# Kernel tuning notes

Measured on AMD Instinct MI355X. Metric: run time of the kernel, lower is better.

The kernel has to match this reference:

```python
import jax, jax.numpy as jnp
import numpy as np

N_NODES = 50000
N_EDGES = 800000
N_FEAT = 16
N_BASIS = 4
GAMMA = 10.0
R_MAX = 5.0
INV_SQRT2 = 0.7071067811865476


def setup_inputs() -> dict:
    key = jax.random.key(0)
    k1, k2, k3, k4 = jax.random.split(key, 4)
    pos = jax.random.normal(k1, (N_NODES, 3), dtype=jnp.float32)
    node_features = jax.random.normal(k2, (N_NODES, N_FEAT), dtype=jnp.float32)
    # build edges with no self-loops: dst = (src + 1 + r) % N, r in [0, N-2]
    src = jax.random.randint(k3, (N_EDGES,), 0, N_NODES)
    r = jax.random.randint(k4, (N_EDGES,), 0, N_NODES - 1)
    dst = (src + 1 + r) % N_NODES
    edge_idx = jnp.stack([src, dst], axis=0).astype(jnp.int64)
    return {"pos": pos, "node_features": node_features, "edge_idx": edge_idx}


def _gaussian_basis(d):
    # d: [E] -> [E, N_BASIS]
    centers = jnp.linspace(0.0, R_MAX, N_BASIS, dtype=d.dtype)
    return jnp.exp(-GAMMA * (d[:, None] - centers[None, :]) ** 2)


def _pos_to_rep(v):
    # v: [N, 3, C] cartesian along axis -2 -> complex spherical l=1 basis,
    # returned as stacked (real, imag): [2, N, 3, C]
    x, y, z = v[..., 0, :], v[..., 1, :], v[..., 2, :]
    zero = jnp.zeros_like(z)
    real = jnp.stack([x * INV_SQRT2, z, -x * INV_SQRT2], axis=-2)
    imag = jnp.stack([-y * INV_SQRT2, zero, -y * INV_SQRT2], axis=-2)
    return jnp.stack([real, imag], axis=0)


def reference(pos, node_features, edge_idx):
    src, dst = edge_idx[0], edge_idx[1]
    disp = pos[dst] - pos[src]                      # [E, 3]
    dist = jnp.linalg.norm(disp, axis=-1)           # [E]
    bf = _gaussian_basis(dist)                      # [E, B]
    unit = disp / dist[:, None]                     # [E, 3]
    nf = node_features[dst]                         # [E, F]
    # outer products: [E, 3, B, F]
    edge_vals = (unit[:, :, None, None] * bf[:, None, :, None]
                 * nf[:, None, None, :])
    edge_vals = edge_vals.reshape(edge_vals.shape[0], 3, N_BASIS * N_FEAT)
    node_vecs = jax.ops.segment_sum(edge_vals, src, num_segments=N_NODES)  # [N,3,C]
    return _pos_to_rep(node_vecs)
```

## Files before the change

kernel.cpp:

```cpp
#include <hip/hip_runtime.h>

#define N_FEAT 16
#define N_BASIS 4
#define GAMMA 10.0f
#define R_MAX 5.0f
#define INV_SQRT2 0.70710678118654752f

#define BUCKET 32
#define CAP 768
#define MAXB 2048
#define SC_BLOCK 512
#define SC_EDGES 4096
#define ACC_BLOCK 512

#define SLOTCAP 1280
#define ROWSTRIDE 1288

#define KC      (-GAMMA * 1.4426950408889634f)
#define CKD     (R_MAX / (N_BASIS - 1))

#if __has_builtin(__builtin_amdgcn_exp2f)
#define EXP2(x) __builtin_amdgcn_exp2f(x)
#else
#define EXP2(x) exp2f(x)
#endif

typedef _Float16 half8 __attribute__((ext_vector_type(8)));
typedef float f32x4 __attribute__((ext_vector_type(4)));

__global__ void bucket_scatter_kernel(const int* __restrict__ src,
                                      const int* __restrict__ dst,
                                      const float* __restrict__ pos,
                                      float4* __restrict__ pos4,
                                      int* __restrict__ gcursor,
                                      int* __restrict__ sorted,
                                      int n_edges, int nbuck, int n_nodes) {
    __shared__ int h[MAXB];
    __shared__ int cur[MAXB];
    __shared__ int gbase[MAXB];
    __shared__ int pay[SC_EDGES];

    int t = threadIdx.x;

    {
        int i = blockIdx.x * SC_BLOCK + t;
        if (i < n_nodes)
            pos4[i] = make_float4(pos[3 * i], pos[3 * i + 1], pos[3 * i + 2], 0.0f);
    }

    int base_e = blockIdx.x * SC_EDGES;
    int nloc = n_edges - base_e;
    if (nloc > SC_EDGES) nloc = SC_EDGES;

    for (int i = t; i < nbuck; i += SC_BLOCK) h[i] = 0;
    __syncthreads();

    unsigned pk[8];
    bool ok[8];
#pragma unroll
    for (int r = 0; r < 8; ++r) {
        int i = t + r * SC_BLOCK;
        ok[r] = (i < nloc);
        unsigned s = ok[r] ? (unsigned)src[base_e + i] : 0u;
        unsigned d = ok[r] ? (unsigned)dst[base_e + i] : 0u;
        pk[r] = (s << 16) | d;
        if (ok[r]) atomicAdd(&h[s >> 5], 1);
    }
    __syncthreads();

    if (t < 64) {
        int run = 0;
        for (int base = 0; base < nbuck; base += 64) {
            int i = base + t;
            int v = (i < nbuck) ? h[i] : 0;
            int incl = v;
            for (int off = 1; off < 64; off <<= 1) {
                int y = __shfl_up(incl, off, 64);
                if (t >= off) incl += y;
            }
            if (i < nbuck) h[i] = run + incl - v;
            run += __shfl(incl, 63, 64);
        }
    }
    __syncthreads();
    for (int i = t; i < nbuck; i += SC_BLOCK) cur[i] = h[i];
    __syncthreads();

#pragma unroll
    for (int r = 0; r < 8; ++r) {
        if (ok[r]) {
            int b = (int)(pk[r] >> 21);
            int p = atomicAdd(&cur[b], 1);
            pay[p] = (int)pk[r];
        }
    }
    __syncthreads();

    for (int b = t; b < nbuck; b += SC_BLOCK) {
        int c = cur[b] - h[b];
        gbase[b] = (c > 0) ? atomicAdd(&gcursor[b], c) : 0;
    }
    __syncthreads();

    for (int i = t; i < nloc; i += SC_BLOCK) {
        unsigned P = (unsigned)pay[i];
        int b = (int)(P >> 21);
        int idx = gbase[b] + (i - h[b]);
        if (idx < CAP) sorted[b * CAP + idx] = (int)P;
    }
}

__global__ __launch_bounds__(ACC_BLOCK) void accumulate_kernel(
        const float4* __restrict__ pos4,
        const float* __restrict__ nfeat,
        const int* __restrict__ sorted,
        const int* __restrict__ gcursor,
        float* __restrict__ out,
        int n_nodes) {
    __shared__ _Float16 a_lds[12 * ROWSTRIDE];
    __shared__ unsigned short slot_dst[SLOTCAP];
    __shared__ int cnt[BUCKET];
    __shared__ int soff[BUCKET];
    __shared__ int curs[BUCKET];
    __shared__ float4 spos[BUCKET];

    int b = blockIdx.x;
    int t = threadIdx.x;
    int w = t >> 6;
    int lane = t & 63;
    int q = lane >> 4;
    int f = lane & 15;
    int nbase = b << 5;

    int ecnt = gcursor[b];
    if (ecnt > CAP) ecnt = CAP;
    const int* seg = sorted + b * CAP;

    {
        int4 z4 = make_int4(0, 0, 0, 0);
        int4* az = (int4*)a_lds;
        for (int i = t; i < 1932; i += ACC_BLOCK) az[i] = z4;
        int4* sz = (int4*)slot_dst;
        if (t < 160) sz[t] = z4;
    }
    if (t < BUCKET) {
        cnt[t] = 0;
        int gn = nbase + t;
        spos[t] = (gn < n_nodes) ? pos4[gn] : make_float4(0.f, 0.f, 0.f, 0.f);
    }
    __syncthreads();

    for (int i = t; i < ecnt; i += ACC_BLOCK)
        atomicAdd(&cnt[((unsigned)seg[i] >> 16) & 31], 1);
    __syncthreads();

    if (t < BUCKET) {
        int deg = cnt[t];
        int pad = (deg + 31) & ~31;
        int incl = pad;
        for (int o2 = 1; o2 < BUCKET; o2 <<= 1) {
            int y = __shfl_up(incl, o2, 64);
            if (t >= o2) incl += y;
        }
        int excl = incl - pad;
        soff[t] = excl;
        curs[t] = excl;
    }
    __syncthreads();

    if (ecnt > 0) {
        int ecm1 = ecnt - 1;
        int i0 = t, i1 = t + ACC_BLOCK;
        bool v0 = (i0 < ecnt), v1 = (i1 < ecnt);
        unsigned E0 = (unsigned)seg[min(i0, ecm1)];
        unsigned E1 = (unsigned)seg[min(i1, ecm1)];
        int d0 = E0 & 0xFFFF, d1 = E1 & 0xFFFF;
        float4 pd0 = pos4[d0];
        float4 pd1 = pos4[d1];
        int sl0 = (E0 >> 16) & 31, sl1 = (E1 >> 16) & 31;
        int p0 = v0 ? atomicAdd(&curs[sl0], 1) : SLOTCAP;
        int p1 = v1 ? atomicAdd(&curs[sl1], 1) : SLOTCAP;

#define STAGE(P, SL, D, PD)                                            \
        if ((P) < SLOTCAP) {                                           \
            float4 ps = spos[SL];                                      \
            float dx = (PD).x - ps.x, dy = (PD).y - ps.y,              \
                  dz = (PD).z - ps.z;                                  \
            float r2 = dx * dx + dy * dy + dz * dz;                    \
            float inv = __builtin_amdgcn_rsqf(r2);                     \
            float dist = r2 * inv;                                     \
            float ux = dx * inv, uy = dy * inv, uz = dz * inv;         \
            slot_dst[P] = (unsigned short)(D);                         \
            _Float16* ap = a_lds + (P);                                \
            _Pragma("unroll")                                          \
            for (int kk = 0; kk < N_BASIS; ++kk) {                     \
                float ck = (float)kk * CKD;                            \
                float tt = dist - ck;                                  \
                float bb = EXP2(tt * tt * KC);                         \
                ap[kk * ROWSTRIDE]       = (_Float16)(ux * bb);        \
                ap[(4 + kk) * ROWSTRIDE] = (_Float16)(uy * bb);        \
                ap[(8 + kk) * ROWSTRIDE] = (_Float16)(uz * bb);        \
            }                                                          \
        }
        { STAGE(p0, sl0, d0, pd0); }
        if (v1) { STAGE(p1, sl1, d1, pd1); }
#undef STAGE
    }
    __syncthreads();

    int arow = (f < 12) ? f : 11;
    const _Float16* abase = &a_lds[arow * ROWSTRIDE];
#pragma unroll
    for (int half = 0; half < 2; ++half) {
        int nA = (w << 2) + (half << 1);
        int nB = nA + 1;
        int baseA = min(soff[nA], SLOTCAP - 32);
        int baseB = min(soff[nB], SLOTCAP - 32);
        int kA = baseA + (q << 3), kB = baseB + (q << 3);

        half8 aA = *(const half8*)&abase[kA];
        half8 aB = *(const half8*)&abase[kB];
        const unsigned short* dpA = &slot_dst[kA];
        const unsigned short* dpB = &slot_dst[kB];
        half8 bA, bB;
#pragma unroll
        for (int j = 0; j < 8; ++j) bA[j] = (_Float16)nfeat[((int)dpA[j] << 4) + f];
#pragma unroll
        for (int j = 0; j < 8; ++j) bB[j] = (_Float16)nfeat[((int)dpB[j] << 4) + f];

        f32x4 CA = {0.f, 0.f, 0.f, 0.f};
        f32x4 CB = {0.f, 0.f, 0.f, 0.f};
        CA = __builtin_amdgcn_mfma_f32_16x16x32_f16(aA, bA, CA, 0, 0, 0);
        CB = __builtin_amdgcn_mfma_f32_16x16x32_f16(aB, bB, CB, 0, 0, 0);

        int ntA = min((cnt[nA] + 31) >> 5, (SLOTCAP - baseA) >> 5);
        for (int tile = 1; tile < ntA; ++tile) {
            int k0 = baseA + (tile << 5) + (q << 3);
            half8 a = *(const half8*)&abase[k0];
            const unsigned short* dp = &slot_dst[k0];
            half8 bf;
#pragma unroll
            for (int j = 0; j < 8; ++j) bf[j] = (_Float16)nfeat[((int)dp[j] << 4) + f];
            CA = __builtin_amdgcn_mfma_f32_16x16x32_f16(a, bf, CA, 0, 0, 0);
        }
        int ntB = min((cnt[nB] + 31) >> 5, (SLOTCAP - baseB) >> 5);
        for (int tile = 1; tile < ntB; ++tile) {
            int k0 = baseB + (tile << 5) + (q << 3);
            half8 a = *(const half8*)&abase[k0];
            const unsigned short* dp = &slot_dst[k0];
            half8 bf;
#pragma unroll
            for (int j = 0; j < 8; ++j) bf[j] = (_Float16)nfeat[((int)dp[j] << 4) + f];
            CB = __builtin_amdgcn_mfma_f32_16x16x32_f16(a, bf, CB, 0, 0, 0);
        }

#define EPI(NL, C)                                                     \
        {                                                              \
            int gn = nbase + (NL);                                     \
            if (gn < n_nodes) {                                        \
                float* re = out + (size_t)gn * 192;                    \
                float* im = re + (size_t)n_nodes * 192;                \
                _Pragma("unroll")                                      \
                for (int r = 0; r < 4; ++r) {                          \
                    float v = (C)[r];                                  \
                    int o1 = r * 16 + f;                               \
                    if (q == 0) {                                      \
                        float xs = v * INV_SQRT2;                      \
                        re[o1] = xs;                                   \
                        re[128 + o1] = -xs;                            \
                    } else if (q == 1) {                               \
                        float ys = -v * INV_SQRT2;                     \
                        im[o1] = ys;                                   \
                        im[128 + o1] = ys;                             \
                    } else if (q == 2) {                               \
                        re[64 + o1] = v;                               \
                    } else {                                           \
                        im[64 + o1] = 0.0f;                            \
                    }                                                  \
                }                                                      \
            }                                                          \
        }
        EPI(nA, CA);
        EPI(nB, CB);
#undef EPI
    }
}

extern "C" void kernel_launch(void* const* d_in, const int* in_sizes, int n_in,
                              void* d_out, int out_size, void* d_ws, size_t ws_size,
                              hipStream_t stream) {
    const float* pos = (const float*)d_in[0];
    const float* nfeat = (const float*)d_in[1];
    const int* edge_idx = (const int*)d_in[2];

    int n_nodes = in_sizes[0] / 3;
    int n_edges = in_sizes[2] / 2;

    const int* src = edge_idx;
    const int* dst = edge_idx + n_edges;

    float* out = (float*)d_out;
    int nbuck = (n_nodes + BUCKET - 1) >> 5;

    char* ws = (char*)d_ws;
    size_t o = 0;
    auto alloc = [&](size_t bytes) {
        char* p = ws + o;
        o = (o + bytes + 255) & ~(size_t)255;
        return p;
    };
    int* gcursor = (int*)alloc((size_t)nbuck * 4);
    int* sorted  = (int*)alloc((size_t)nbuck * CAP * 4);
    float4* pos4 = (float4*)alloc((size_t)n_nodes * 16);

    (void)hipMemsetAsync(gcursor, 0, (size_t)nbuck * sizeof(int), stream);

    {
        int grid = (n_edges + SC_EDGES - 1) / SC_EDGES;
        bucket_scatter_kernel<<<grid, SC_BLOCK, 0, stream>>>(src, dst, pos, pos4,
                                                             gcursor, sorted,
                                                             n_edges, nbuck, n_nodes);
    }

    accumulate_kernel<<<nbuck, ACC_BLOCK, 0, stream>>>(pos4, nfeat, sorted, gcursor,
                                                       out, n_nodes);
}
```

Before: 59.18 us.

## Pre-convert node features to fp16 and make accumulate kernel persistent

The scatter kernel now also converts node features to an fp16 copy in workspace, so the accumulate kernel's gathers read 2-byte values and skip the per-element float-to-half conversion. The accumulate kernel becomes a grid-stride persistent loop over buckets with a fixed grid of 1024 blocks, adding a trailing barrier per iteration so the shared buffers can be reused. This halves gather traffic for the B operand at the cost of an extra write and read pass over the features, and it reduces block launch overhead but may cut latency hiding when fewer blocks are resident.

```diff
diff --git a/kernel.cpp b/kernel.cpp
--- a/kernel.cpp
+++ b/kernel.cpp
@@ -12,6 +12,7 @@
 #define SC_BLOCK 512
 #define SC_EDGES 4096
 #define ACC_BLOCK 512
+#define ACC_GRID 1024
 
 #define SLOTCAP 1280
 #define ROWSTRIDE 1288
@@ -31,7 +32,9 @@
 __global__ void bucket_scatter_kernel(const int* __restrict__ src,
                                       const int* __restrict__ dst,
                                       const float* __restrict__ pos,
+                                      const float* __restrict__ nfeat,
                                       float4* __restrict__ pos4,
+                                      _Float16* __restrict__ nf16,
                                       int* __restrict__ gcursor,
                                       int* __restrict__ sorted,
                                       int n_edges, int nbuck, int n_nodes) {
@@ -44,8 +47,23 @@
 
     {
         int i = blockIdx.x * SC_BLOCK + t;
-        if (i < n_nodes)
+        if (i < n_nodes) {
             pos4[i] = make_float4(pos[3 * i], pos[3 * i + 1], pos[3 * i + 2], 0.0f);
+            const float4* nfs = (const float4*)(nfeat + ((size_t)i << 4));
+            half8 lo, hi;
+            float4 v0 = nfs[0], v1 = nfs[1], v2 = nfs[2], v3 = nfs[3];
+            lo[0] = (_Float16)v0.x; lo[1] = (_Float16)v0.y;
+            lo[2] = (_Float16)v0.z; lo[3] = (_Float16)v0.w;
+            lo[4] = (_Float16)v1.x; lo[5] = (_Float16)v1.y;
+            lo[6] = (_Float16)v1.z; lo[7] = (_Float16)v1.w;
+            hi[0] = (_Float16)v2.x; hi[1] = (_Float16)v2.y;
+            hi[2] = (_Float16)v2.z; hi[3] = (_Float16)v2.w;
+            hi[4] = (_Float16)v3.x; hi[5] = (_Float16)v3.y;
+            hi[6] = (_Float16)v3.z; hi[7] = (_Float16)v3.w;
+            half8* dst16 = (half8*)(nf16 + ((size_t)i << 4));
+            dst16[0] = lo;
+            dst16[1] = hi;
+        }
     }
 
     int base_e = blockIdx.x * SC_EDGES;
@@ -112,11 +130,11 @@
 
 __global__ __launch_bounds__(ACC_BLOCK) void accumulate_kernel(
         const float4* __restrict__ pos4,
-        const float* __restrict__ nfeat,
+        const _Float16* __restrict__ nf16,
         const int* __restrict__ sorted,
         const int* __restrict__ gcursor,
         float* __restrict__ out,
-        int n_nodes) {
+        int n_nodes, int nbuck) {
     __shared__ _Float16 a_lds[12 * ROWSTRIDE];
     __shared__ unsigned short slot_dst[SLOTCAP];
     __shared__ int cnt[BUCKET];
@@ -124,165 +142,167 @@
     __shared__ int curs[BUCKET];
     __shared__ float4 spos[BUCKET];
 
-    int b = blockIdx.x;
     int t = threadIdx.x;
     int w = t >> 6;
     int lane = t & 63;
     int q = lane >> 4;
     int f = lane & 15;
-    int nbase = b << 5;
-
-    int ecnt = gcursor[b];
-    if (ecnt > CAP) ecnt = CAP;
-    const int* seg = sorted + b * CAP;
-
-    {
-        int4 z4 = make_int4(0, 0, 0, 0);
-        int4* az = (int4*)a_lds;
-        for (int i = t; i < 1932; i += ACC_BLOCK) az[i] = z4;
-        int4* sz = (int4*)slot_dst;
-        if (t < 160) sz[t] = z4;
-    }
-    if (t < BUCKET) {
-        cnt[t] = 0;
-        int gn = nbase + t;
-        spos[t] = (gn < n_nodes) ? pos4[gn] : make_float4(0.f, 0.f, 0.f, 0.f);
-    }
-    __syncthreads();
-
-    for (int i = t; i < ecnt; i += ACC_BLOCK)
-        atomicAdd(&cnt[((unsigned)seg[i] >> 16) & 31], 1);
-    __syncthreads();
-
-    if (t < BUCKET) {
-        int deg = cnt[t];
-        int pad = (deg + 31) & ~31;
-        int incl = pad;
-        for (int o2 = 1; o2 < BUCKET; o2 <<= 1) {
-            int y = __shfl_up(incl, o2, 64);
-            if (t >= o2) incl += y;
-        }
-        int excl = incl - pad;
-        soff[t] = excl;
-        curs[t] = excl;
-    }
-    __syncthreads();
-
-    if (ecnt > 0) {
-        int ecm1 = ecnt - 1;
-        int i0 = t, i1 = t + ACC_BLOCK;
-        bool v0 = (i0 < ecnt), v1 = (i1 < ecnt);
-        unsigned E0 = (unsigned)seg[min(i0, ecm1)];
-        unsigned E1 = (unsigned)seg[min(i1, ecm1)];
-        int d0 = E0 & 0xFFFF, d1 = E1 & 0xFFFF;
-        float4 pd0 = pos4[d0];
-        float4 pd1 = pos4[d1];
-        int sl0 = (E0 >> 16) & 31, sl1 = (E1 >> 16) & 31;
-        int p0 = v0 ? atomicAdd(&curs[sl0], 1) : SLOTCAP;
-        int p1 = v1 ? atomicAdd(&curs[sl1], 1) : SLOTCAP;
+    int arow = (f < 12) ? f : 11;
+
+    for (int b = blockIdx.x; b < nbuck; b += ACC_GRID) {
+        int nbase = b << 5;
+        int ecnt = gcursor[b];
+        if (ecnt > CAP) ecnt = CAP;
+        const int* seg = sorted + b * CAP;
+
+        {
+            int4 z4 = make_int4(0, 0, 0, 0);
+            int4* az = (int4*)a_lds;
+            for (int i = t; i < 1932; i += ACC_BLOCK) az[i] = z4;
+            int4* sz = (int4*)slot_dst;
+            if (t < 160) sz[t] = z4;
+        }
+        if (t < BUCKET) {
+            cnt[t] = 0;
+            int gn = nbase + t;
+            spos[t] = (gn < n_nodes) ? pos4[gn] : make_float4(0.f, 0.f, 0.f, 0.f);
+        }
+        __syncthreads();
+
+        for (int i = t; i < ecnt; i += ACC_BLOCK)
+            atomicAdd(&cnt[((unsigned)seg[i] >> 16) & 31], 1);
+        __syncthreads();
+
+        if (t < BUCKET) {
+            int deg = cnt[t];
+            int pad = (deg + 31) & ~31;
+            int incl = pad;
+            for (int o2 = 1; o2 < BUCKET; o2 <<= 1) {
+                int y = __shfl_up(incl, o2, 64);
+                if (t >= o2) incl += y;
+            }
+            int excl = incl - pad;
+            soff[t] = excl;
+            curs[t] = excl;
+        }
+        __syncthreads();
+
+        if (ecnt > 0) {
+            int ecm1 = ecnt - 1;
+            int i0 = t, i1 = t + ACC_BLOCK;
+            bool v0 = (i0 < ecnt), v1 = (i1 < ecnt);
+            unsigned E0 = (unsigned)seg[min(i0, ecm1)];
+            unsigned E1 = (unsigned)seg[min(i1, ecm1)];
+            int d0 = E0 & 0xFFFF, d1 = E1 & 0xFFFF;
+            float4 pd0 = pos4[d0];
+            float4 pd1 = pos4[d1];
+            int sl0 = (E0 >> 16) & 31, sl1 = (E1 >> 16) & 31;
+            int p0 = v0 ? atomicAdd(&curs[sl0], 1) : SLOTCAP;
+            int p1 = v1 ? atomicAdd(&curs[sl1], 1) : SLOTCAP;
 
 #define STAGE(P, SL, D, PD)                                            \
-        if ((P) < SLOTCAP) {                                           \
-            float4 ps = spos[SL];                                      \
-            float dx = (PD).x - ps.x, dy = (PD).y - ps.y,              \
-                  dz = (PD).z - ps.z;                                  \
-            float r2 = dx * dx + dy * dy + dz * dz;                    \
-            float inv = __builtin_amdgcn_rsqf(r2);                     \
-            float dist = r2 * inv;                                     \
-            float ux = dx * inv, uy = dy * inv, uz = dz * inv;         \
-            slot_dst[P] = (unsigned short)(D);                         \
-            _Float16* ap = a_lds + (P);                                \
-            _Pragma("unroll")                                          \
-            for (int kk = 0; kk < N_BASIS; ++kk) {                     \
-                float ck = (float)kk * CKD;                            \
-                float tt = dist - ck;                                  \
-                float bb = EXP2(tt * tt * KC);                         \
-                ap[kk * ROWSTRIDE]       = (_Float16)(ux * bb);        \
-                ap[(4 + kk) * ROWSTRIDE] = (_Float16)(uy * bb);        \
-                ap[(8 + kk) * ROWSTRIDE] = (_Float16)(uz * bb);        \
-            }                                                          \
-        }
-        { STAGE(p0, sl0, d0, pd0); }
-        if (v1) { STAGE(p1, sl1, d1, pd1); }
+            if ((P) < SLOTCAP) {                                       \
+                float4 ps = spos[SL];                                  \
+                float dx = (PD).x - ps.x, dy = (PD).y - ps.y,          \
+                      dz = (PD).z - ps.z;                              \
+                float r2 = dx * dx + dy * dy + dz * dz;                \
+                float inv = __builtin_amdgcn_rsqf(r2);                 \
+                float dist = r2 * inv;                                 \
+                float ux = dx * inv, uy = dy * inv, uz = dz * inv;     \
+                slot_dst[P] = (unsigned short)(D);                     \
+                _Float16* ap = a_lds + (P);                            \
+                _Pragma("unroll")                                      \
+                for (int kk = 0; kk < N_BASIS; ++kk) {                 \
+                    float ck = (float)kk * CKD;                        \
+                    float tt = dist - ck;                              \
+                    float bb = EXP2(tt * tt * KC);                     \
+                    ap[kk * ROWSTRIDE]       = (_Float16)(ux * bb);    \
+                    ap[(4 + kk) * ROWSTRIDE] = (_Float16)(uy * bb);    \
+                    ap[(8 + kk) * ROWSTRIDE] = (_Float16)(uz * bb);    \
+                }                                                      \
+            }
+            { STAGE(p0, sl0, d0, pd0); }
+            if (v1) { STAGE(p1, sl1, d1, pd1); }
 #undef STAGE
-    }
-    __syncthreads();
-
-    int arow = (f < 12) ? f : 11;
-    const _Float16* abase = &a_lds[arow * ROWSTRIDE];
-#pragma unroll
-    for (int half = 0; half < 2; ++half) {
-        int nA = (w << 2) + (half << 1);
-        int nB = nA + 1;
-        int baseA = min(soff[nA], SLOTCAP - 32);
-        int baseB = min(soff[nB], SLOTCAP - 32);
-        int kA = baseA + (q << 3), kB = baseB + (q << 3);
-
-        half8 aA = *(const half8*)&abase[kA];
-        half8 aB = *(const half8*)&abase[kB];
-        const unsigned short* dpA = &slot_dst[kA];
-        const unsigned short* dpB = &slot_dst[kB];
-        half8 bA, bB;
-#pragma unroll
-        for (int j = 0; j < 8; ++j) bA[j] = (_Float16)nfeat[((int)dpA[j] << 4) + f];
-#pragma unroll
-        for (int j = 0; j < 8; ++j) bB[j] = (_Float16)nfeat[((int)dpB[j] << 4) + f];
-
-        f32x4 CA = {0.f, 0.f, 0.f, 0.f};
-        f32x4 CB = {0.f, 0.f, 0.f, 0.f};
-        CA = __builtin_amdgcn_mfma_f32_16x16x32_f16(aA, bA, CA, 0, 0, 0);
-        CB = __builtin_amdgcn_mfma_f32_16x16x32_f16(aB, bB, CB, 0, 0, 0);
-
-        int ntA = min((cnt[nA] + 31) >> 5, (SLOTCAP - baseA) >> 5);
-        for (int tile = 1; tile < ntA; ++tile) {
-            int k0 = baseA + (tile << 5) + (q << 3);
-            half8 a = *(const half8*)&abase[k0];
-            const unsigned short* dp = &slot_dst[k0];
-            half8 bf;
-#pragma unroll
-            for (int j = 0; j < 8; ++j) bf[j] = (_Float16)nfeat[((int)dp[j] << 4) + f];
-            CA = __builtin_amdgcn_mfma_f32_16x16x32_f16(a, bf, CA, 0, 0, 0);
-        }
-        int ntB = min((cnt[nB] + 31) >> 5, (SLOTCAP - baseB) >> 5);
-        for (int tile = 1; tile < ntB; ++tile) {
-            int k0 = baseB + (tile << 5) + (q << 3);
-            half8 a = *(const half8*)&abase[k0];
-            const unsigned short* dp = &slot_dst[k0];
-            half8 bf;
-#pragma unroll
-            for (int j = 0; j < 8; ++j) bf[j] = (_Float16)nfeat[((int)dp[j] << 4) + f];
-            CB = __builtin_amdgcn_mfma_f32_16x16x32_f16(a, bf, CB, 0, 0, 0);
-        }
+        }
+        __syncthreads();
+
+        const _Float16* abase = &a_lds[arow * ROWSTRIDE];
+#pragma unroll
+        for (int half = 0; half < 2; ++half) {
+            int nA = (w << 2) + (half << 1);
+            int nB = nA + 1;
+            int baseA = min(soff[nA], SLOTCAP - 32);
+            int baseB = min(soff[nB], SLOTCAP - 32);
+            int kA = baseA + (q << 3), kB = baseB + (q << 3);
+
+            half8 aA = *(const half8*)&abase[kA];
+            half8 aB = *(const half8*)&abase[kB];
+            const unsigned short* dpA = &slot_dst[kA];
+            const unsigned short* dpB = &slot_dst[kB];
+            half8 bA, bB;
+#pragma unroll
+            for (int j = 0; j < 8; ++j) bA[j] = nf16[((int)dpA[j] << 4) + f];
+#pragma unroll
+            for (int j = 0; j < 8; ++j) bB[j] = nf16[((int)dpB[j] << 4) + f];
+
+            f32x4 CA = {0.f, 0.f, 0.f, 0.f};
+            f32x4 CB = {0.f, 0.f, 0.f, 0.f};
+            CA = __builtin_amdgcn_mfma_f32_16x16x32_f16(aA, bA, CA, 0, 0, 0);
+            CB = __builtin_amdgcn_mfma_f32_16x16x32_f16(aB, bB, CB, 0, 0, 0);
+
+            int ntA = min((cnt[nA] + 31) >> 5, (SLOTCAP - baseA) >> 5);
+            for (int tile = 1; tile < ntA; ++tile) {
+                int k0 = baseA + (tile << 5) + (q << 3);
+                half8 a = *(const half8*)&abase[k0];
+                const unsigned short* dp = &slot_dst[k0];
+                half8 bf;
+#pragma unroll
+                for (int j = 0; j < 8; ++j) bf[j] = nf16[((int)dp[j] << 4) + f];
+                CA = __builtin_amdgcn_mfma_f32_16x16x32_f16(a, bf, CA, 0, 0, 0);
+            }
+            int ntB = min((cnt[nB] + 31) >> 5, (SLOTCAP - baseB) >> 5);
+            for (int tile = 1; tile < ntB; ++tile) {
+                int k0 = baseB + (tile << 5) + (q << 3);
+                half8 a = *(const half8*)&abase[k0];
+                const unsigned short* dp = &slot_dst[k0];
+                half8 bf;
+#pragma unroll
+                for (int j = 0; j < 8; ++j) bf[j] = nf16[((int)dp[j] << 4) + f];
+                CB = __builtin_amdgcn_mfma_f32_16x16x32_f16(a, bf, CB, 0, 0, 0);
+            }
 
 #define EPI(NL, C)                                                     \
-        {                                                              \
-            int gn = nbase + (NL);                                     \
-            if (gn < n_nodes) {                                        \
-                float* re = out + (size_t)gn * 192;                    \
-                float* im = re + (size_t)n_nodes * 192;                \
-                _Pragma("unroll")                                      \
-                for (int r = 0; r < 4; ++r) {                          \
-                    float v = (C)[r];                                  \
-                    int o1 = r * 16 + f;                               \
-                    if (q == 0) {                                      \
-                        float xs = v * INV_SQRT2;                      \
-                        re[o1] = xs;                                   \
-                        re[128 + o1] = -xs;                            \
-                    } else if (q == 1) {                               \
-                        float ys = -v * INV_SQRT2;                     \
-                        im[o1] = ys;                                   \
-                        im[128 + o1] = ys;                             \
-                    } else if (q == 2) {                               \
-                        re[64 + o1] = v;                               \
-                    } else {                                           \
-                        im[64 + o1] = 0.0f;                            \
+            {                                                          \
+                int gn = nbase + (NL);                                 \
+                if (gn < n_nodes) {                                    \
+                    float* re = out + (size_t)gn * 192;                \
+                    float* im = re + (size_t)n_nodes * 192;            \
+                    _Pragma("unroll")                                  \
+                    for (int r = 0; r < 4; ++r) {                      \
+                        float v = (C)[r];                              \
+                        int o1 = r * 16 + f;                           \
+                        if (q == 0) {                                  \
+                            float xs = v * INV_SQRT2;                  \
+                            re[o1] = xs;                               \
+                            re[128 + o1] = -xs;                        \
+                        } else if (q == 1) {                           \
+                            float ys = -v * INV_SQRT2;                 \
+                            im[o1] = ys;                               \
+                            im[128 + o1] = ys;                         \
+                        } else if (q == 2) {                           \
+                            re[64 + o1] = v;                           \
+                        } else {                                       \
+                            im[64 + o1] = 0.0f;                        \
+                        }                                              \
                     }                                                  \
                 }                                                      \
-            }                                                          \
-        }
-        EPI(nA, CA);
-        EPI(nB, CB);
+            }
+            EPI(nA, CA);
+            EPI(nB, CB);
 #undef EPI
+        }
+        __syncthreads();
     }
 }
 
@@ -309,19 +329,24 @@
         o = (o + bytes + 255) & ~(size_t)255;
         return p;
     };
-    int* gcursor = (int*)alloc((size_t)nbuck * 4);
-    int* sorted  = (int*)alloc((size_t)nbuck * CAP * 4);
-    float4* pos4 = (float4*)alloc((size_t)n_nodes * 16);
+    int* gcursor   = (int*)alloc((size_t)nbuck * 4);
+    int* sorted    = (int*)alloc((size_t)nbuck * CAP * 4);
+    float4* pos4   = (float4*)alloc((size_t)n_nodes * 16);
+    _Float16* nf16 = (_Float16*)alloc((size_t)n_nodes * 32);
 
     (void)hipMemsetAsync(gcursor, 0, (size_t)nbuck * sizeof(int), stream);
 
     {
         int grid = (n_edges + SC_EDGES - 1) / SC_EDGES;
-        bucket_scatter_kernel<<<grid, SC_BLOCK, 0, stream>>>(src, dst, pos, pos4,
+        bucket_scatter_kernel<<<grid, SC_BLOCK, 0, stream>>>(src, dst, pos, nfeat,
+                                                             pos4, nf16,
                                                              gcursor, sorted,
                                                              n_edges, nbuck, n_nodes);
     }
 
-    accumulate_kernel<<<nbuck, ACC_BLOCK, 0, stream>>>(pos4, nfeat, sorted, gcursor,
-                                                       out, n_nodes);
+    {
+        int grid = (nbuck < ACC_GRID) ? nbuck : ACC_GRID;
+        accumulate_kernel<<<grid, ACC_BLOCK, 0, stream>>>(pos4, nf16, sorted, gcursor,
+                                                          out, n_nodes, nbuck);
+    }
 }
```

Result: no change. 58.93 us (-0.4%).
